# Performance work log

Hardware: AMD Instinct MI355X
Metric: run time of the kernel (lower is better)

## Reference

```python
import math
import jax, jax.numpy as jnp
import numpy as np

CHANNELS = 512
OUT_CHANNELS = 512
N_HEADS = 8
K_CHANNELS = CHANNELS // N_HEADS
WINDOW = 4


def _get_relative_embeddings(emb, length):
    # emb: [1, 2*WINDOW+1, d] -> [1, 2*length-1, d]
    max_rel = 2 * WINDOW + 1
    pad_length = max(0, length - (WINDOW + 1))
    start = max(0, WINDOW + 1 - length)
    end = max_rel + 2 * length - 1
    if pad_length > 0:
        emb = jnp.pad(emb, ((0, 0), (pad_length, pad_length), (0, 0)))
    return emb[:, start:end]


def _rel_to_abs(x):
    # x: [b, h, l, 2l-1] -> [b, h, l, l] via skewing trick
    b, h, l, _ = x.shape
    x = jnp.pad(x, ((0, 0), (0, 0), (0, 0), (0, 1)))
    x_flat = x.reshape(b, h, l * 2 * l)
    x_flat = jnp.pad(x_flat, ((0, 0), (0, 0), (0, l - 1)))
    return x_flat.reshape(b, h, l + 1, 2 * l - 1)[..., :l, l - 1:]


def _abs_to_rel(x):
    # x: [b, h, l, l] -> [b, h, l, 2l-1]
    b, h, l, _ = x.shape
    x = jnp.pad(x, ((0, 0), (0, 0), (0, 0), (0, l - 1)))
    x_flat = x.reshape(b, h, -1)
    x_flat = jnp.pad(x_flat, ((0, 0), (0, 0), (l, 0)))
    return x_flat.reshape(b, h, l, 2 * l)[..., 1:]


def setup_inputs() -> dict:
    key = jax.random.key(0)
    ks = jax.random.split(key, 12)
    B, T = 4, 1024
    w_std = 1.0 / math.sqrt(CHANNELS)
    rel_std = K_CHANNELS ** (-0.5)
    return {
        'x': jax.random.normal(ks[0], (B, T, CHANNELS), jnp.float32),
        'c': jax.random.normal(ks[1], (B, T, CHANNELS), jnp.float32),
        'Wq': jax.random.normal(ks[2], (CHANNELS, CHANNELS), jnp.float32) * w_std,
        'bq': jnp.zeros((CHANNELS,), jnp.float32),
        'Wk': jax.random.normal(ks[3], (CHANNELS, CHANNELS), jnp.float32) * w_std,
        'bk': jnp.zeros((CHANNELS,), jnp.float32),
        'Wv': jax.random.normal(ks[4], (CHANNELS, CHANNELS), jnp.float32) * w_std,
        'bv': jnp.zeros((CHANNELS,), jnp.float32),
        'Wo': jax.random.normal(ks[5], (CHANNELS, OUT_CHANNELS), jnp.float32) * w_std,
        'bo': jnp.zeros((OUT_CHANNELS,), jnp.float32),
        'emb_rel_k': jax.random.normal(ks[6], (1, 2 * WINDOW + 1, K_CHANNELS), jnp.float32) * rel_std,
        'emb_rel_v': jax.random.normal(ks[7], (1, 2 * WINDOW + 1, K_CHANNELS), jnp.float32) * rel_std,
    }


def reference(x, c, Wq, bq, Wk, bk, Wv, bv, Wo, bo, emb_rel_k, emb_rel_v):
    b, t_t, _ = x.shape
    t_s = c.shape[1]
    # 1x1 convs == pointwise dense projections
    q = x @ Wq + bq
    k = c @ Wk + bk
    v = c @ Wv + bv
    q = q.reshape(b, t_t, N_HEADS, K_CHANNELS).transpose(0, 2, 1, 3)
    k = k.reshape(b, t_s, N_HEADS, K_CHANNELS).transpose(0, 2, 1, 3)
    v = v.reshape(b, t_s, N_HEADS, K_CHANNELS).transpose(0, 2, 1, 3)
    q_scaled = q / math.sqrt(K_CHANNELS)
    scores = jnp.einsum('bhtd,bhsd->bhts', q_scaled, k)
    # relative position bias via skewing trick (heads_share=True -> rel emb head dim 1)
    rel_k = _get_relative_embeddings(emb_rel_k, t_s)[0]  # [2*t_s-1, d]
    rel_logits = jnp.einsum('bhtd,md->bhtm', q_scaled, rel_k)
    scores = scores + _rel_to_abs(rel_logits)
    p_attn = jax.nn.softmax(scores, axis=-1)
    out = jnp.einsum('bhts,bhsd->bhtd', p_attn, v)
    rel_w = _abs_to_rel(p_attn)  # [b, h, t, 2t-1]
    rel_v = _get_relative_embeddings(emb_rel_v, t_s)[0]  # [2*t_s-1, d]
    out = out + jnp.einsum('bhtm,md->bhtd', rel_w, rel_v)
    out = out.transpose(0, 2, 1, 3).reshape(b, t_t, CHANNELS)
    return out @ Wo + bo
```

## Files before the change

kernel.cpp:

```cpp
#include <hip/hip_runtime.h>
#include <hip/hip_bf16.h>

#define B_ 4
#define T_ 1024
#define C_ 512
#define H_ 8

typedef __attribute__((ext_vector_type(8))) short short8;
typedef __attribute__((ext_vector_type(4))) float floatx4;

__device__ __forceinline__ unsigned short f2bs(float f) {
    __hip_bfloat16 h = __float2bfloat16(f);
    return *(unsigned short*)&h;
}
__device__ __forceinline__ float bs2f(unsigned short u) {
    __hip_bfloat16 h;
    *(unsigned short*)&h = u;
    return __bfloat162float(h);
}

__device__ __forceinline__ void gload_lds16(const void* g, void* l) {
    __builtin_amdgcn_global_load_lds(
        (const __attribute__((address_space(1))) unsigned int*)g,
        (__attribute__((address_space(3))) unsigned int*)l, 16, 0, 0);
}

__global__ __launch_bounds__(256) void prep(
    const float* __restrict__ x, const float* __restrict__ c,
    const float* __restrict__ Wq, const float* __restrict__ Wk,
    const float* __restrict__ Wv, const float* __restrict__ Wo,
    unsigned short* __restrict__ xb, unsigned short* __restrict__ cb,
    unsigned short* __restrict__ WT)
{
    __shared__ unsigned short tileT[32][33];
    const int bx = blockIdx.x, tid = threadIdx.x;
    if (bx < 2048) {
        const float* src = (bx < 1024) ? x : c;
        unsigned short* dst = (bx < 1024) ? xb : cb;
        const size_t base = (size_t)(bx & 1023) * 2048 + (size_t)tid * 8;
        const float4 a = *(const float4*)&src[base];
        const float4 b = *(const float4*)&src[base + 4];
        short8 o;
        o[0] = (short)f2bs(a.x); o[1] = (short)f2bs(a.y);
        o[2] = (short)f2bs(a.z); o[3] = (short)f2bs(a.w);
        o[4] = (short)f2bs(b.x); o[5] = (short)f2bs(b.y);
        o[6] = (short)f2bs(b.z); o[7] = (short)f2bs(b.w);
        *(short8*)&dst[base] = o;
    } else {
        const int r = bx - 2048;
        const int w = r >> 8, tile = r & 255;
        const int k0 = (tile >> 4) * 32, n0 = (tile & 15) * 32;
        const float* W = (w == 0) ? Wq : (w == 1) ? Wk : (w == 2) ? Wv : Wo;
        unsigned short* out = WT + (size_t)w * 512 * 512;
        const int kk = tid >> 3, ns = (tid & 7) * 4;
        const float4 v = *(const float4*)&W[(size_t)(k0 + kk) * 512 + n0 + ns];
        tileT[ns + 0][kk] = f2bs(v.x);
        tileT[ns + 1][kk] = f2bs(v.y);
        tileT[ns + 2][kk] = f2bs(v.z);
        tileT[ns + 3][kk] = f2bs(v.w);
        __syncthreads();
        const int nn = tid >> 3, ks = (tid & 7) * 4;
        ushort4 o;
        o.x = tileT[nn][ks + 0]; o.y = tileT[nn][ks + 1];
        o.z = tileT[nn][ks + 2]; o.w = tileT[nn][ks + 3];
        *(ushort4*)&out[(size_t)(n0 + nn) * 512 + k0 + ks] = o;
    }
}

struct GemmAcc { floatx4 acc[4][4]; int mrow, kgrp, mhalf, nhalf; };

__device__ __forceinline__ void gemm_core(
    const unsigned short* __restrict__ A, const unsigned short* __restrict__ Bt,
    int m0, int n0, unsigned short* sA, unsigned short* sB, GemmAcc& g)
{
    const int tid = threadIdx.x;
    const int wave = tid >> 6, lane = tid & 63;
    g.mrow = lane & 15;
    g.kgrp = (lane >> 4) * 8;
    g.mhalf = (wave & 1) * 64;
    g.nhalf = (wave >> 1) * 64;
    const int lrow = lane >> 2;
    const int lseg = (lane & 3) * 16;
    const int srow = wave * 32;

    #pragma unroll
    for (int i = 0; i < 4; i++)
        #pragma unroll
        for (int j = 0; j < 4; j++)
            g.acc[i][j] = (floatx4){0.f, 0.f, 0.f, 0.f};

    for (int ck = 0; ck < 16; ck++) {
        const int k0 = ck * 32;
        __syncthreads();
        #pragma unroll
        for (int j = 0; j < 2; j++) {
            const int rA = srow + j * 16 + lrow;
            gload_lds16((const char*)A + ((size_t)(m0 + rA) * 512 + k0) * 2 + lseg,
                        &sA[(size_t)(srow + j * 16) * 32]);
            gload_lds16((const char*)Bt + ((size_t)(n0 + rA) * 512 + k0) * 2 + lseg,
                        &sB[(size_t)(srow + j * 16) * 32]);
        }
        __syncthreads();
        short8 af[4], bf[4];
        #pragma unroll
        for (int i = 0; i < 4; i++)
            af[i] = *(const short8*)&sA[(size_t)(g.mhalf + i * 16 + g.mrow) * 32 + g.kgrp];
        #pragma unroll
        for (int i = 0; i < 4; i++)
            bf[i] = *(const short8*)&sB[(size_t)(g.nhalf + i * 16 + g.mrow) * 32 + g.kgrp];
        #pragma unroll
        for (int mt = 0; mt < 4; mt++)
            #pragma unroll
            for (int nt = 0; nt < 4; nt++)
                g.acc[mt][nt] = __builtin_amdgcn_mfma_f32_16x16x32_bf16(
                    af[mt], bf[nt], g.acc[mt][nt], 0, 0, 0);
    }
}

__global__ __launch_bounds__(256) void qkv_mfma(
    const unsigned short* __restrict__ xb, const unsigned short* __restrict__ cb,
    const unsigned short* __restrict__ WT,
    const float* __restrict__ bq, const float* __restrict__ bk,
    const float* __restrict__ bv,
    unsigned short* __restrict__ Qc, unsigned short* __restrict__ Kc,
    unsigned short* __restrict__ Vtg)
{
    const int z = blockIdx.z;
    const unsigned short* A  = (z == 0) ? xb : cb;
    const unsigned short* Bt = WT + (size_t)z * 262144;
    const float* bias        = (z == 0) ? bq : (z == 1) ? bk : bv;
    const float scale        = (z == 0) ? 0.125f : 1.0f;

    __shared__ __align__(16) unsigned short sA[128 * 32];
    __shared__ __align__(16) unsigned short sB[128 * 32];

    const int m0 = blockIdx.y * 128, n0 = blockIdx.x * 128;
    GemmAcc g;
    gemm_core(A, Bt, m0, n0, sA, sB, g);

    const int lane = threadIdx.x & 63;
    const int rowq = (lane >> 4) * 4;
    if (z < 2) {
        unsigned short* Y = (z == 0) ? Qc : Kc;
        #pragma unroll
        for (int nt = 0; nt < 4; nt++) {
            const int n = n0 + g.nhalf + nt * 16 + g.mrow;
            const float bv_ = bias[n];
            const int h = n >> 6, d = n & 63;
            #pragma unroll
            for (int mt = 0; mt < 4; mt++)
                #pragma unroll
                for (int r = 0; r < 4; r++) {
                    const int m = m0 + g.mhalf + mt * 16 + rowq + r;
                    const int bb = m >> 10, t = m & 1023;
                    Y[(((size_t)bb * H_ + h) * 1024 + t) * 64 + d] =
                        f2bs((g.acc[mt][nt][r] + bv_) * scale);
                }
        }
    } else {
        #pragma unroll
        for (int nt = 0; nt < 4; nt++) {
            const int n = n0 + g.nhalf + nt * 16 + g.mrow;
            const float bv_ = bias[n];
            const int h = n >> 6, d = n & 63;
            #pragma unroll
            for (int mt = 0; mt < 4; mt++) {
                const int m = m0 + g.mhalf + mt * 16 + rowq;
                const int bb = m >> 10, t = m & 1023;
                ushort4 o4;
                o4.x = f2bs(g.acc[mt][nt][0] + bv_);
                o4.y = f2bs(g.acc[mt][nt][1] + bv_);
                o4.z = f2bs(g.acc[mt][nt][2] + bv_);
                o4.w = f2bs(g.acc[mt][nt][3] + bv_);
                *(ushort4*)&Vtg[(((size_t)bb * H_ + h) * 64 + d) * 1024 + t] = o4;
            }
        }
    }
}

__global__ __launch_bounds__(256) void out_mfma(
    const unsigned short* __restrict__ AOb, const unsigned short* __restrict__ WoT,
    const float* __restrict__ bias, float* __restrict__ out)
{
    __shared__ __align__(16) unsigned short sA[128 * 32];
    __shared__ __align__(16) unsigned short sB[128 * 32];

    const int m0 = blockIdx.y * 128, n0 = blockIdx.x * 128;
    GemmAcc g;
    gemm_core(AOb, WoT, m0, n0, sA, sB, g);

    const int lane = threadIdx.x & 63;
    const int rowq = (lane >> 4) * 4;
    #pragma unroll
    for (int nt = 0; nt < 4; nt++) {
        const int n = n0 + g.nhalf + nt * 16 + g.mrow;
        const float bv_ = bias[n];
        #pragma unroll
        for (int mt = 0; mt < 4; mt++)
            #pragma unroll
            for (int r = 0; r < 4; r++) {
                const int m = m0 + g.mhalf + mt * 16 + rowq + r;
                out[(size_t)m * 512 + n] = g.acc[mt][nt][r] + bv_;
            }
    }
}

__global__ __launch_bounds__(256) void attn_mfma(
    const unsigned short* __restrict__ Qc, const unsigned short* __restrict__ Kc,
    const unsigned short* __restrict__ Vtg,
    const float* __restrict__ rk,
    unsigned short* __restrict__ Opart, float* __restrict__ lpart,
    float* __restrict__ bandP)
{
    __shared__ __align__(16) unsigned short KL[64 * 64];
    __shared__ __align__(16) unsigned short VtL[64 * 64];
    __shared__ __align__(16) unsigned short PL[4][16 * 72];
    __shared__ float qbL[64 * 9];

    const int tb = blockIdx.x, sh = blockIdx.y, bh = blockIdx.z;
    const int tid = threadIdx.x;
    const int wave = tid >> 6, lane = tid & 63;
    const int t0 = tb * 64;
    const int t0w = t0 + wave * 16;
    const size_t qkbase = (size_t)bh * T_ * 64;
    const size_t vtbase = (size_t)bh * 64 * T_;

    for (int idx = tid; idx < 576; idx += 256) {
        const int row = idx / 9, w = idx - row * 9;
        const unsigned short* qp = &Qc[qkbase + (size_t)(t0 + row) * 64];
        float s = 0.f;
        #pragma unroll
        for (int d8 = 0; d8 < 8; d8++) {
            const short8 q8 = *(const short8*)&qp[d8 * 8];
            #pragma unroll
            for (int i = 0; i < 8; i++)
                s = fmaf(bs2f((unsigned short)q8[i]), rk[w * 64 + d8 * 8 + i], s);
        }
        qbL[idx] = s;
    }

    const int mrow = lane & 15;
    const int quad = lane >> 4;
    const int kgrp = quad * 8;
    const int x7 = mrow & 7;

    const int ldrow = lane >> 3;
    const int gseg = (lane & 7) ^ ldrow;

    const short8 aQ0 = *(const short8*)&Qc[qkbase + (size_t)(t0w + mrow) * 64 + kgrp];
    const short8 aQ1 = *(const short8*)&Qc[qkbase + (size_t)(t0w + mrow) * 64 + 32 + kgrp];

    floatx4 Oc[4];
    float ls[4] = {0.f, 0.f, 0.f, 0.f};
    #pragma unroll
    for (int dt = 0; dt < 4; dt++) Oc[dt] = (floatx4){0.f, 0.f, 0.f, 0.f};

    unsigned short* Pw = &PL[wave][0];
    float* qbw = &qbL[wave * 16 * 9];

    for (int ck = 0; ck < 8; ck++) {
        const int s0 = sh * 512 + ck * 64;
        __syncthreads();
        #pragma unroll
        for (int j = 0; j < 2; j++) {
            const int br = wave * 16 + j * 8;
            gload_lds16((const char*)Kc + (qkbase + (size_t)(s0 + br + ldrow) * 64) * 2 + gseg * 16,
                        &KL[br * 64]);
            gload_lds16((const char*)Vtg + (vtbase + (size_t)(br + ldrow) * 1024 + s0) * 2 + gseg * 16,
                        &VtL[br * 64]);
        }
        __syncthreads();

        floatx4 Sc[4];
        #pragma unroll
        for (int st = 0; st < 4; st++) {
            const int row = st * 16 + mrow;
            const short8 bK0 = *(const short8*)&KL[row * 64 + ((quad) ^ x7) * 8];
            const short8 bK1 = *(const short8*)&KL[row * 64 + ((4 + quad) ^ x7) * 8];
            floatx4 s4 = {0.f, 0.f, 0.f, 0.f};
            s4 = __builtin_amdgcn_mfma_f32_16x16x32_bf16(aQ0, bK0, s4, 0, 0, 0);
            s4 = __builtin_amdgcn_mfma_f32_16x16x32_bf16(aQ1, bK1, s4, 0, 0, 0);
            Sc[st] = s4;
        }

        #pragma unroll
        for (int st = 0; st < 4; st++) {
            #pragma unroll
            for (int r = 0; r < 4; r++) {
                const int tloc = quad * 4 + r;
                const int rel = (s0 + st * 16 + mrow) - (t0w + tloc);
                float sc = Sc[st][r];
                const bool inband = (rel >= -4) && (rel <= 4);
                if (inband) sc += qbw[tloc * 9 + rel + 4];
                const float p = __expf(sc);
                if (inband)
                    bandP[((size_t)bh * 1024 + t0w + tloc) * 9 + rel + 4] = p;
                Pw[tloc * 72 + st * 16 + mrow] = f2bs(p);
                ls[r] += p;
            }
        }

        #pragma unroll
        for (int c = 0; c < 2; c++) {
            const short8 aP = *(const short8*)&Pw[mrow * 72 + c * 32 + kgrp];
            #pragma unroll
            for (int dt = 0; dt < 4; dt++) {
                const int segl = (c * 4 + quad) ^ x7;
                const short8 bV = *(const short8*)&VtL[(dt * 16 + mrow) * 64 + segl * 8];
                Oc[dt] = __builtin_amdgcn_mfma_f32_16x16x32_bf16(aP, bV, Oc[dt], 0, 0, 0);
            }
        }
    }

    float lsum[4];
    #pragma unroll
    for (int r = 0; r < 4; r++) {
        float v = ls[r];
        #pragma unroll
        for (int mk = 1; mk < 16; mk <<= 1)
            v += __shfl_xor(v, mk);
        lsum[r] = v;
    }
    if (mrow == 0) {
        #pragma unroll
        for (int r = 0; r < 4; r++)
            lpart[((size_t)sh * 32 + bh) * 1024 + t0w + quad * 4 + r] = lsum[r];
    }

    const size_t ob = (((size_t)sh * 32 + bh) * 1024 + t0w) * 64;
    #pragma unroll
    for (int dt = 0; dt < 4; dt++)
        #pragma unroll
        for (int r = 0; r < 4; r++)
            Opart[ob + (size_t)(quad * 4 + r) * 64 + dt * 16 + mrow] = f2bs(Oc[dt][r]);
}

__global__ __launch_bounds__(256) void combine(
    const unsigned short* __restrict__ Opart, const float* __restrict__ lpart,
    const float* __restrict__ bandP, const float* __restrict__ rv,
    unsigned short* __restrict__ AOb)
{
    const int bh = blockIdx.y;
    const int b = bh >> 3, h = bh & 7;
    const int tid = threadIdx.x;
    const int tr = tid >> 6, d = tid & 63;
    const int t = blockIdx.x * 4 + tr;

    const size_t i0 = ((size_t)bh * 1024 + t) * 64 + d;
    const size_t half = (size_t)32 * 1024 * 64;
    float o = bs2f(Opart[i0]) + bs2f(Opart[half + i0]);
    const float l = lpart[(size_t)bh * 1024 + t] + lpart[(size_t)32 * 1024 + bh * 1024 + t];
    const float inv = 1.f / l;
    o *= inv;
    #pragma unroll
    for (int w = 0; w < 9; w++) {
        const int s = t + w - 4;
        if (s >= 0 && s < 1024)
            o = fmaf(bandP[((size_t)bh * 1024 + t) * 9 + w] * inv, rv[w * 64 + d], o);
    }
    AOb[((size_t)b * 1024 + t) * 512 + h * 64 + d] = f2bs(o);
}

extern "C" void kernel_launch(void* const* d_in, const int* in_sizes, int n_in,
                              void* d_out, int out_size, void* d_ws, size_t ws_size,
                              hipStream_t stream)
{
    const float* x  = (const float*)d_in[0];
    const float* c  = (const float*)d_in[1];
    const float* Wq = (const float*)d_in[2];
    const float* bq = (const float*)d_in[3];
    const float* Wk = (const float*)d_in[4];
    const float* bk = (const float*)d_in[5];
    const float* Wv = (const float*)d_in[6];
    const float* bv = (const float*)d_in[7];
    const float* Wo = (const float*)d_in[8];
    const float* bo = (const float*)d_in[9];
    const float* rk = (const float*)d_in[10];
    const float* rv = (const float*)d_in[11];

    unsigned short* xb  = (unsigned short*)d_ws;
    unsigned short* cb  = xb + (size_t)4096 * 512;
    unsigned short* WT  = cb + (size_t)4096 * 512;
    unsigned short* Qc  = WT + (size_t)4 * 512 * 512;
    unsigned short* Kc  = Qc + (size_t)32 * 1024 * 64;
    unsigned short* Vtg = Kc + (size_t)32 * 1024 * 64;
    unsigned short* AOb = Vtg + (size_t)32 * 1024 * 64;
    float* lpart = (float*)(AOb + (size_t)4096 * 512);
    float* bandP = lpart + (size_t)2 * 32 * 1024;
    unsigned short* Opart = xb;

    prep<<<3072, 256, 0, stream>>>(x, c, Wq, Wk, Wv, Wo, xb, cb, WT);
    qkv_mfma<<<dim3(4, 32, 3), 256, 0, stream>>>(xb, cb, WT, bq, bk, bv, Qc, Kc, Vtg);
    attn_mfma<<<dim3(16, 2, 32), 256, 0, stream>>>(Qc, Kc, Vtg, rk, Opart, lpart, bandP);
    combine<<<dim3(256, 32), 256, 0, stream>>>(Opart, lpart, bandP, rv, AOb);
    out_mfma<<<dim3(4, 32), 256, 0, stream>>>(AOb, WT + (size_t)3 * 262144, bo, (float*)d_out);
}
```

Measured before the change: 177.0 us.

## Double-buffer LDS tiles in GEMM and attention kernels, narrow output GEMM tiles

The GEMM core and the attention K/V loop now use two LDS buffers. The next chunk's global-to-LDS loads are issued before computing on the current chunk, and each iteration keeps only one barrier instead of two. This aims to hide global load latency behind the MFMA work, at the cost of doubled LDS footprint, which can lower occupancy. The attention softmax loop also skips the relative-band check and the bandP stores for 16-column tiles that lie far from the diagonal. The output projection switches to 128x64 tiles, giving twice as many blocks on the device.

```diff
diff --git a/kernel.cpp b/kernel.cpp
--- a/kernel.cpp
+++ b/kernel.cpp
@@ -67,53 +67,80 @@
     }
 }
 
-struct GemmAcc { floatx4 acc[4][4]; int mrow, kgrp, mhalf, nhalf; };
-
-__device__ __forceinline__ void gemm_core(
+template <int BROWS>
+__device__ __forceinline__ void gemm_stage(
     const unsigned short* __restrict__ A, const unsigned short* __restrict__ Bt,
-    int m0, int n0, unsigned short* sA, unsigned short* sB, GemmAcc& g)
-{
+    int m0, int n0, int k0, int wave, int lrow, int lseg,
+    unsigned short* sAb, unsigned short* sBb)
+{
+    #pragma unroll
+    for (int j = 0; j < 2; j++) {
+        const int rA = wave * 32 + j * 16 + lrow;
+        gload_lds16((const char*)A + ((size_t)(m0 + rA) * 512 + k0) * 2 + lseg,
+                    &sAb[(size_t)(wave * 32 + j * 16) * 32]);
+    }
+    if constexpr (BROWS == 128) {
+        #pragma unroll
+        for (int j = 0; j < 2; j++) {
+            const int rB = wave * 32 + j * 16 + lrow;
+            gload_lds16((const char*)Bt + ((size_t)(n0 + rB) * 512 + k0) * 2 + lseg,
+                        &sBb[(size_t)(wave * 32 + j * 16) * 32]);
+        }
+    } else {
+        const int rB = wave * 16 + lrow;
+        gload_lds16((const char*)Bt + ((size_t)(n0 + rB) * 512 + k0) * 2 + lseg,
+                    &sBb[(size_t)(wave * 16) * 32]);
+    }
+}
+
+template <int NT>
+struct GemmAccT { floatx4 acc[4][NT]; int mrow, kgrp, mhalf, noff; };
+
+template <int NT>
+__device__ __forceinline__ void gemm_coreT(
+    const unsigned short* __restrict__ A, const unsigned short* __restrict__ Bt,
+    int m0, int n0, unsigned short* sA, unsigned short* sB, GemmAccT<NT>& g)
+{
+    constexpr int BROWS = NT * 32;
     const int tid = threadIdx.x;
     const int wave = tid >> 6, lane = tid & 63;
     g.mrow = lane & 15;
     g.kgrp = (lane >> 4) * 8;
     g.mhalf = (wave & 1) * 64;
-    g.nhalf = (wave >> 1) * 64;
+    g.noff = (wave >> 1) * (NT * 16);
     const int lrow = lane >> 2;
     const int lseg = (lane & 3) * 16;
-    const int srow = wave * 32;
 
     #pragma unroll
     for (int i = 0; i < 4; i++)
         #pragma unroll
-        for (int j = 0; j < 4; j++)
+        for (int j = 0; j < NT; j++)
             g.acc[i][j] = (floatx4){0.f, 0.f, 0.f, 0.f};
 
+    gemm_stage<BROWS>(A, Bt, m0, n0, 0, wave, lrow, lseg, sA, sB);
+
     for (int ck = 0; ck < 16; ck++) {
-        const int k0 = ck * 32;
+        const int buf = ck & 1;
         __syncthreads();
-        #pragma unroll
-        for (int j = 0; j < 2; j++) {
-            const int rA = srow + j * 16 + lrow;
-            gload_lds16((const char*)A + ((size_t)(m0 + rA) * 512 + k0) * 2 + lseg,
-                        &sA[(size_t)(srow + j * 16) * 32]);
-            gload_lds16((const char*)Bt + ((size_t)(n0 + rA) * 512 + k0) * 2 + lseg,
-                        &sB[(size_t)(srow + j * 16) * 32]);
-        }
-        __syncthreads();
-        short8 af[4], bf[4];
+        if (ck < 15)
+            gemm_stage<BROWS>(A, Bt, m0, n0, (ck + 1) * 32, wave, lrow, lseg,
+                              sA + (size_t)(buf ^ 1) * 128 * 32,
+                              sB + (size_t)(buf ^ 1) * BROWS * 32);
+        const unsigned short* sAb = sA + (size_t)buf * 128 * 32;
+        const unsigned short* sBb = sB + (size_t)buf * BROWS * 32;
+        short8 af[4], bfv[NT];
         #pragma unroll
         for (int i = 0; i < 4; i++)
-            af[i] = *(const short8*)&sA[(size_t)(g.mhalf + i * 16 + g.mrow) * 32 + g.kgrp];
-        #pragma unroll
-        for (int i = 0; i < 4; i++)
-            bf[i] = *(const short8*)&sB[(size_t)(g.nhalf + i * 16 + g.mrow) * 32 + g.kgrp];
+            af[i] = *(const short8*)&sAb[(size_t)(g.mhalf + i * 16 + g.mrow) * 32 + g.kgrp];
+        #pragma unroll
+        for (int i = 0; i < NT; i++)
+            bfv[i] = *(const short8*)&sBb[(size_t)(g.noff + i * 16 + g.mrow) * 32 + g.kgrp];
         #pragma unroll
         for (int mt = 0; mt < 4; mt++)
             #pragma unroll
-            for (int nt = 0; nt < 4; nt++)
+            for (int nt = 0; nt < NT; nt++)
                 g.acc[mt][nt] = __builtin_amdgcn_mfma_f32_16x16x32_bf16(
-                    af[mt], bf[nt], g.acc[mt][nt], 0, 0, 0);
+                    af[mt], bfv[nt], g.acc[mt][nt], 0, 0, 0);
     }
 }
 
@@ -131,12 +158,12 @@
     const float* bias        = (z == 0) ? bq : (z == 1) ? bk : bv;
     const float scale        = (z == 0) ? 0.125f : 1.0f;
 
-    __shared__ __align__(16) unsigned short sA[128 * 32];
-    __shared__ __align__(16) unsigned short sB[128 * 32];
+    __shared__ __align__(16) unsigned short sA[2 * 128 * 32];
+    __shared__ __align__(16) unsigned short sB[2 * 128 * 32];
 
     const int m0 = blockIdx.y * 128, n0 = blockIdx.x * 128;
-    GemmAcc g;
-    gemm_core(A, Bt, m0, n0, sA, sB, g);
+    GemmAccT<4> g;
+    gemm_coreT<4>(A, Bt, m0, n0, sA, sB, g);
 
     const int lane = threadIdx.x & 63;
     const int rowq = (lane >> 4) * 4;
@@ -144,7 +171,7 @@
         unsigned short* Y = (z == 0) ? Qc : Kc;
         #pragma unroll
         for (int nt = 0; nt < 4; nt++) {
-            const int n = n0 + g.nhalf + nt * 16 + g.mrow;
+            const int n = n0 + g.noff + nt * 16 + g.mrow;
             const float bv_ = bias[n];
             const int h = n >> 6, d = n & 63;
             #pragma unroll
@@ -160,7 +187,7 @@
     } else {
         #pragma unroll
         for (int nt = 0; nt < 4; nt++) {
-            const int n = n0 + g.nhalf + nt * 16 + g.mrow;
+            const int n = n0 + g.noff + nt * 16 + g.mrow;
             const float bv_ = bias[n];
             const int h = n >> 6, d = n & 63;
             #pragma unroll
@@ -182,18 +209,18 @@
     const unsigned short* __restrict__ AOb, const unsigned short* __restrict__ WoT,
     const float* __restrict__ bias, float* __restrict__ out)
 {
-    __shared__ __align__(16) unsigned short sA[128 * 32];
-    __shared__ __align__(16) unsigned short sB[128 * 32];
-
-    const int m0 = blockIdx.y * 128, n0 = blockIdx.x * 128;
-    GemmAcc g;
-    gemm_core(AOb, WoT, m0, n0, sA, sB, g);
+    __shared__ __align__(16) unsigned short sA[2 * 128 * 32];
+    __shared__ __align__(16) unsigned short sB[2 * 64 * 32];
+
+    const int m0 = blockIdx.y * 128, n0 = blockIdx.x * 64;
+    GemmAccT<2> g;
+    gemm_coreT<2>(AOb, WoT, m0, n0, sA, sB, g);
 
     const int lane = threadIdx.x & 63;
     const int rowq = (lane >> 4) * 4;
     #pragma unroll
-    for (int nt = 0; nt < 4; nt++) {
-        const int n = n0 + g.nhalf + nt * 16 + g.mrow;
+    for (int nt = 0; nt < 2; nt++) {
+        const int n = n0 + g.noff + nt * 16 + g.mrow;
         const float bv_ = bias[n];
         #pragma unroll
         for (int mt = 0; mt < 4; mt++)
@@ -202,6 +229,21 @@
                 const int m = m0 + g.mhalf + mt * 16 + rowq + r;
                 out[(size_t)m * 512 + n] = g.acc[mt][nt][r] + bv_;
             }
+    }
+}
+
+__device__ __forceinline__ void attn_stage(
+    const unsigned short* __restrict__ Kc, const unsigned short* __restrict__ Vtg,
+    size_t qkbase, size_t vtbase, int s0, int wave, int ldrow, int gseg,
+    unsigned short* KLb, unsigned short* VtLb)
+{
+    #pragma unroll
+    for (int j = 0; j < 2; j++) {
+        const int br = wave * 16 + j * 8;
+        gload_lds16((const char*)Kc + (qkbase + (size_t)(s0 + br + ldrow) * 64) * 2 + gseg * 16,
+                    &KLb[br * 64]);
+        gload_lds16((const char*)Vtg + (vtbase + (size_t)(br + ldrow) * 1024 + s0) * 2 + gseg * 16,
+                    &VtLb[br * 64]);
     }
 }
 
@@ -212,8 +254,8 @@
     unsigned short* __restrict__ Opart, float* __restrict__ lpart,
     float* __restrict__ bandP)
 {
-    __shared__ __align__(16) unsigned short KL[64 * 64];
-    __shared__ __align__(16) unsigned short VtL[64 * 64];
+    __shared__ __align__(16) unsigned short KL[2][64 * 64];
+    __shared__ __align__(16) unsigned short VtL[2][64 * 64];
     __shared__ __align__(16) unsigned short PL[4][16 * 72];
     __shared__ float qbL[64 * 9];
 
@@ -225,6 +267,16 @@
     const size_t qkbase = (size_t)bh * T_ * 64;
     const size_t vtbase = (size_t)bh * 64 * T_;
 
+    const int mrow = lane & 15;
+    const int quad = lane >> 4;
+    const int kgrp = quad * 8;
+    const int x7 = mrow & 7;
+    const int ldrow = lane >> 3;
+    const int gseg = (lane & 7) ^ ldrow;
+
+    attn_stage(Kc, Vtg, qkbase, vtbase, sh * 512, wave, ldrow, gseg,
+               &KL[0][0], &VtL[0][0]);
+
     for (int idx = tid; idx < 576; idx += 256) {
         const int row = idx / 9, w = idx - row * 9;
         const unsigned short* qp = &Qc[qkbase + (size_t)(t0 + row) * 64];
@@ -239,14 +291,6 @@
         qbL[idx] = s;
     }
 
-    const int mrow = lane & 15;
-    const int quad = lane >> 4;
-    const int kgrp = quad * 8;
-    const int x7 = mrow & 7;
-
-    const int ldrow = lane >> 3;
-    const int gseg = (lane & 7) ^ ldrow;
-
     const short8 aQ0 = *(const short8*)&Qc[qkbase + (size_t)(t0w + mrow) * 64 + kgrp];
     const short8 aQ1 = *(const short8*)&Qc[qkbase + (size_t)(t0w + mrow) * 64 + 32 + kgrp];
 
@@ -260,23 +304,18 @@
 
     for (int ck = 0; ck < 8; ck++) {
         const int s0 = sh * 512 + ck * 64;
+        const int buf = ck & 1;
         __syncthreads();
-        #pragma unroll
-        for (int j = 0; j < 2; j++) {
-            const int br = wave * 16 + j * 8;
-            gload_lds16((const char*)Kc + (qkbase + (size_t)(s0 + br + ldrow) * 64) * 2 + gseg * 16,
-                        &KL[br * 64]);
-            gload_lds16((const char*)Vtg + (vtbase + (size_t)(br + ldrow) * 1024 + s0) * 2 + gseg * 16,
-                        &VtL[br * 64]);
-        }
-        __syncthreads();
+        if (ck < 7)
+            attn_stage(Kc, Vtg, qkbase, vtbase, s0 + 64, wave, ldrow, gseg,
+                       &KL[buf ^ 1][0], &VtL[buf ^ 1][0]);
 
         floatx4 Sc[4];
         #pragma unroll
         for (int st = 0; st < 4; st++) {
             const int row = st * 16 + mrow;
-            const short8 bK0 = *(const short8*)&KL[row * 64 + ((quad) ^ x7) * 8];
-            const short8 bK1 = *(const short8*)&KL[row * 64 + ((4 + quad) ^ x7) * 8];
+            const short8 bK0 = *(const short8*)&KL[buf][row * 64 + (quad ^ x7) * 8];
+            const short8 bK1 = *(const short8*)&KL[buf][row * 64 + ((4 + quad) ^ x7) * 8];
             floatx4 s4 = {0.f, 0.f, 0.f, 0.f};
             s4 = __builtin_amdgcn_mfma_f32_16x16x32_bf16(aQ0, bK0, s4, 0, 0, 0);
             s4 = __builtin_amdgcn_mfma_f32_16x16x32_bf16(aQ1, bK1, s4, 0, 0, 0);
@@ -285,18 +324,29 @@
 
         #pragma unroll
         for (int st = 0; st < 4; st++) {
-            #pragma unroll
-            for (int r = 0; r < 4; r++) {
-                const int tloc = quad * 4 + r;
-                const int rel = (s0 + st * 16 + mrow) - (t0w + tloc);
-                float sc = Sc[st][r];
-                const bool inband = (rel >= -4) && (rel <= 4);
-                if (inband) sc += qbw[tloc * 9 + rel + 4];
-                const float p = __expf(sc);
-                if (inband)
-                    bandP[((size_t)bh * 1024 + t0w + tloc) * 9 + rel + 4] = p;
-                Pw[tloc * 72 + st * 16 + mrow] = f2bs(p);
-                ls[r] += p;
+            const int diff = s0 + st * 16 - t0w;
+            if (diff >= -19 && diff <= 19) {
+                #pragma unroll
+                for (int r = 0; r < 4; r++) {
+                    const int tloc = quad * 4 + r;
+                    const int rel = diff + mrow - tloc;
+                    float sc = Sc[st][r];
+                    const bool inband = (rel >= -4) && (rel <= 4);
+                    if (inband) sc += qbw[tloc * 9 + rel + 4];
+                    const float p = __expf(sc);
+                    if (inband)
+                        bandP[((size_t)bh * 1024 + t0w + tloc) * 9 + rel + 4] = p;
+                    Pw[tloc * 72 + st * 16 + mrow] = f2bs(p);
+                    ls[r] += p;
+                }
+            } else {
+                #pragma unroll
+                for (int r = 0; r < 4; r++) {
+                    const int tloc = quad * 4 + r;
+                    const float p = __expf(Sc[st][r]);
+                    Pw[tloc * 72 + st * 16 + mrow] = f2bs(p);
+                    ls[r] += p;
+                }
             }
         }
 
@@ -306,7 +356,7 @@
             #pragma unroll
             for (int dt = 0; dt < 4; dt++) {
                 const int segl = (c * 4 + quad) ^ x7;
-                const short8 bV = *(const short8*)&VtL[(dt * 16 + mrow) * 64 + segl * 8];
+                const short8 bV = *(const short8*)&VtL[buf][(dt * 16 + mrow) * 64 + segl * 8];
                 Oc[dt] = __builtin_amdgcn_mfma_f32_16x16x32_bf16(aP, bV, Oc[dt], 0, 0, 0);
             }
         }
@@ -393,5 +443,5 @@
     qkv_mfma<<<dim3(4, 32, 3), 256, 0, stream>>>(xb, cb, WT, bq, bk, bv, Qc, Kc, Vtg);
     attn_mfma<<<dim3(16, 2, 32), 256, 0, stream>>>(Qc, Kc, Vtg, rk, Opart, lpart, bandP);
     combine<<<dim3(256, 32), 256, 0, stream>>>(Opart, lpart, bandP, rv, AOb);
-    out_mfma<<<dim3(4, 32), 256, 0, stream>>>(AOb, WT + (size_t)3 * 262144, bo, (float*)d_out);
-}
+    out_mfma<<<dim3(8, 32), 256, 0, stream>>>(AOb, WT + (size_t)3 * 262144, bo, (float*)d_out);
+}
```

New measurement: 175.9 us. Within noise of the previous version (-0.6%).
